# Kernel tuning notes

Hardware: AMD Instinct MI355X
Metric: run time of the kernel (lower is better)

## Reference

```python
import jax, jax.numpy as jnp
import numpy as np

H = 16      # n_heads
DK = 64     # d_k = d_v = input_dim // n_heads
D = 1024    # input_dim = ouput_dim


def setup_inputs() -> dict:
    key = jax.random.key(0)
    ks = jax.random.split(key, 10)
    s = 1.0 / np.float32(np.sqrt(D))
    inp = {
        'X':  jax.random.normal(ks[0], (2048, D), jnp.float32),
        'X1': jax.random.normal(ks[1], (3072, D), jnp.float32),
        'WQ':  jax.random.normal(ks[2], (D, H * DK), jnp.float32) * s,
        'WK':  jax.random.normal(ks[3], (D, H * DK), jnp.float32) * s,
        'WV':  jax.random.normal(ks[4], (D, H * DK), jnp.float32) * s,
        'WQ1': jax.random.normal(ks[5], (D, H * DK), jnp.float32) * s,
        'WK1': jax.random.normal(ks[6], (D, H * DK), jnp.float32) * s,
        'WV1': jax.random.normal(ks[7], (D, H * DK), jnp.float32) * s,
        'Wfc':  jax.random.normal(ks[8], (H * DK, D), jnp.float32) * s,
        'Wfc1': jax.random.normal(ks[9], (H * DK, D), jnp.float32) * s,
    }
    return inp


def _heads(x):
    # [N, H*DK] -> [H, N, DK]  (matches .view(-1,H,DK).transpose(0,1))
    return x.reshape(-1, H, DK).transpose(1, 0, 2)


def reference(X, X1, WQ, WK, WV, WQ1, WK1, WV1, Wfc, Wfc1):
    scale = jnp.float32(1.0 / np.sqrt(DK))
    Q,  K,  V  = _heads(X @ WQ),  _heads(X @ WK),  _heads(X @ WV)   # [H,N,DK]
    Q1, K1, V1 = _heads(X1 @ WQ1), _heads(X1 @ WK1), _heads(X1 @ WV1)  # [H,N1,DK]

    # direction 1: queries from X1 attend over X
    scores = jnp.einsum('hqd,hkd->hqk', Q1, K) * scale           # [H,N1,N]
    attn = jax.nn.softmax(scores, axis=-1)
    context = jnp.einsum('hqk,hkd->hqd', attn, V)                # [H,N1,DK]

    # direction 2: queries from X attend over X1
    scores1 = jnp.einsum('hqd,hkd->hqk', Q, K1) * scale          # [H,N,N1]
    attn1 = jax.nn.softmax(scores1, axis=-1)
    context1 = jnp.einsum('hqk,hkd->hqd', attn1, V1)             # [H,N,DK]

    # faithful to torch: .transpose(1,2).reshape(-1, H*DK) (head/len axes interleaved)
    context = context.transpose(0, 2, 1).reshape(-1, H * DK)     # [N1, H*DK] rows
    context1 = context1.transpose(0, 2, 1).reshape(-1, H * DK)   # [N,  H*DK] rows

    output = context @ Wfc     # [N1, D]
    output1 = context1 @ Wfc1  # [N,  D]
    return (output, output1)
```

## Files before the change

kernel.cpp:

```cpp
#include <hip/hip_runtime.h>
#include <stdint.h>

typedef unsigned short u16;
typedef unsigned int u32;
typedef u16   u16x4  __attribute__((ext_vector_type(4)));
typedef u16   u16x8  __attribute__((ext_vector_type(8)));
typedef short s16x4  __attribute__((ext_vector_type(4)));
typedef __bf16 bf16x4 __attribute__((ext_vector_type(4)));
typedef __bf16 bf16x8 __attribute__((ext_vector_type(8)));
typedef float f32x4  __attribute__((ext_vector_type(4)));
typedef u32   u32x2  __attribute__((ext_vector_type(2)));

typedef __attribute__((address_space(3))) u16 lds_u16;
typedef __attribute__((address_space(1))) const u16 glb_u16;

static __device__ __forceinline__ u16 f32_bf16(float f) {
    uint32_t u = __builtin_bit_cast(uint32_t, f);
    u += 0x7fffu + ((u >> 16) & 1u);
    return (u16)(u >> 16);
}
static __device__ __forceinline__ u32 pack_bf16(float a, float b) {
    return (u32)f32_bf16(a) | ((u32)f32_bf16(b) << 16);
}
static __device__ __forceinline__ u16x8 cvt8(f32x4 a, f32x4 b) {
    u16x8 v;
#pragma unroll
    for (int e = 0; e < 4; ++e) { v[e] = f32_bf16(a[e]); v[4 + e] = f32_bf16(b[e]); }
    return v;
}

static __device__ __forceinline__ f32x4 mfma16(u32x2 a, u32x2 b, f32x4 c) {
#if __has_builtin(__builtin_amdgcn_mfma_f32_16x16x16_bf16)
    return __builtin_amdgcn_mfma_f32_16x16x16_bf16(
        __builtin_bit_cast(bf16x4, a), __builtin_bit_cast(bf16x4, b), c, 0, 0, 0);
#elif __has_builtin(__builtin_amdgcn_mfma_f32_16x16x16bf16_1k)
    return __builtin_amdgcn_mfma_f32_16x16x16bf16_1k(
        __builtin_bit_cast(s16x4, a), __builtin_bit_cast(s16x4, b), c, 0, 0, 0);
#else
    f32x4 d;
    asm volatile("v_mfma_f32_16x16x16_bf16 %0, %1, %2, %3"
                 : "=v"(d) : "v"(a), "v"(b), "v"(c));
    return d;
#endif
}

__global__ __launch_bounds__(256) void detect_k(const u16* __restrict__ X, uint32_t* flag) {
    __shared__ int cnt[256];
    int t = threadIdx.x;
    int c = 0;
#pragma unroll
    for (int i = 0; i < 4; ++i) {
        u16 v = X[t + 256 * i];
        int e = (v >> 7) & 0xFF;
        c += (e >= 0xC2) ? 1 : 0;
    }
    cnt[t] = c;
    __syncthreads();
    for (int s = 128; s > 0; s >>= 1) {
        if (t < s) cnt[t] += cnt[t + s];
        __syncthreads();
    }
    if (t == 0) *flag = (cnt[0] > 32) ? 1u : 0u;
}

struct XJob { const void* in; u16* out; int n; };

__global__ __launch_bounds__(256) void convert_x(XJob j0, XJob j1, const uint32_t* __restrict__ flag) {
    const XJob job = (blockIdx.y == 0) ? j0 : j1;
    const bool f32in = (*flag != 0u);
    const int stride = gridDim.x * 256 * 8;
    for (int i = ((int)blockIdx.x * 256 + (int)threadIdx.x) * 8; i < job.n; i += stride) {
        u16x8 v;
        if (f32in) {
            const float* p = (const float*)job.in + i;
            v = cvt8(*(const f32x4*)p, *(const f32x4*)(p + 4));
        } else {
            v = *(const u16x8*)((const u16*)job.in + i);
        }
        *(u16x8*)(job.out + i) = v;
    }
}

struct WJob { const void* in; u16* out; };
struct WBatch8 { WJob j[8]; };

__global__ __launch_bounds__(256) void convert_w(WBatch8 args, const uint32_t* __restrict__ flag) {
    __shared__ u16 tile[64][72];
    const bool f32in = (*flag != 0u);
    const void* in = args.j[blockIdx.z].in;
    u16*       out = args.j[blockIdx.z].out;
    const int t  = threadIdx.x;
    const int r0 = blockIdx.y * 64, c0 = blockIdx.x * 64;
    const int lr = t >> 3, lc = (t & 7) * 8;
#pragma unroll
    for (int pass = 0; pass < 2; ++pass) {
        int r = lr + pass * 32;
        u16x8 v;
        if (f32in) {
            const float* p = (const float*)in + (size_t)(r0 + r) * 1024 + c0 + lc;
            v = cvt8(*(const f32x4*)p, *(const f32x4*)(p + 4));
        } else {
            v = *(const u16x8*)((const u16*)in + (size_t)(r0 + r) * 1024 + c0 + lc);
        }
#pragma unroll
        for (int e = 0; e < 8; ++e) tile[r][lc + e] = v[e];
    }
    __syncthreads();
#pragma unroll
    for (int pass = 0; pass < 2; ++pass) {
        int n = lr + pass * 32;
        u16x8 v;
#pragma unroll
        for (int e = 0; e < 8; ++e) v[e] = tile[lc + e][n];
        *(u16x8*)(out + (size_t)(c0 + n) * 1024 + r0 + lc) = v;
    }
}

struct GemmJob  { const u16* A; const u16* Bt; void* C; int M; int cF32able; int cOffElems; int vtNk; };
struct GemmBatch6 { GemmJob j[6]; };

__global__ __launch_bounds__(256) void gemm_bt(GemmBatch6 b, const uint32_t* __restrict__ flag) {
    const GemmJob job = b.j[blockIdx.z];
    const int K = 1024, N = 1024;
    const int m0 = blockIdx.y * 128;
    if (m0 >= job.M) return;
    const int n0 = blockIdx.x * 128;
    const bool cF = job.cF32able && (*flag != 0u);

    __shared__ u16 As[128 * 64];
    __shared__ u16 Bs[128 * 64];

    const int tid  = threadIdx.x;
    const int lane = tid & 63, wave = tid >> 6;
    const int quad = lane >> 4, l16 = lane & 15;
    const int wrow = wave >> 1, wcol = wave & 1;

    f32x4 acc[4][4];
#pragma unroll
    for (int i = 0; i < 4; ++i)
#pragma unroll
        for (int j = 0; j < 4; ++j) acc[i][j] = (f32x4){0.f, 0.f, 0.f, 0.f};

    for (int k0 = 0; k0 < K; k0 += 64) {
        __syncthreads();
#pragma unroll
        for (int i = 0; i < 4; ++i) {
            int id = tid + 256 * i;
            int row = id >> 3, slot = id & 7;
            int src = (slot ^ (row & 7)) * 8;
            __builtin_amdgcn_global_load_lds(
                (glb_u16*)(job.A + (size_t)(m0 + row) * K + k0 + src),
                (lds_u16*)(As + (size_t)id * 8), 16, 0, 0);
            __builtin_amdgcn_global_load_lds(
                (glb_u16*)(job.Bt + (size_t)(n0 + row) * K + k0 + src),
                (lds_u16*)(Bs + (size_t)id * 8), 16, 0, 0);
        }
        __syncthreads();

#pragma unroll
        for (int kc2 = 0; kc2 < 2; ++kc2) {
            bf16x8 af[4], bfb[4];
#pragma unroll
            for (int i = 0; i < 4; ++i) {
                int r  = wrow * 64 + i * 16 + l16;
                af[i]  = *(const bf16x8*)(As + r * 64 + (((kc2 * 4 + quad) ^ (r & 7)) * 8));
                int rn = wcol * 64 + i * 16 + l16;
                bfb[i] = *(const bf16x8*)(Bs + rn * 64 + (((kc2 * 4 + quad) ^ (rn & 7)) * 8));
            }
#pragma unroll
            for (int i = 0; i < 4; ++i)
#pragma unroll
                for (int j = 0; j < 4; ++j)
                    acc[i][j] = __builtin_amdgcn_mfma_f32_16x16x32_bf16(af[i], bfb[j], acc[i][j], 0, 0, 0);
        }
    }

    if (job.vtNk > 0) {
        u16* VT = (u16*)job.C;
        const int Nk2 = job.vtNk;
#pragma unroll
        for (int i = 0; i < 4; ++i)
#pragma unroll
            for (int j = 0; j < 4; ++j) {
                int n   = n0 + wcol * 64 + j * 16 + l16;
                int hh  = n >> 6, dd = n & 63;
                int key = m0 + wrow * 64 + i * 16 + quad * 4;
                u16x4 vv;
#pragma unroll
                for (int r = 0; r < 4; ++r) vv[r] = f32_bf16(acc[i][j][r]);
                *(u16x4*)(VT + (size_t)hh * 64 * Nk2 + (size_t)dd * Nk2 + key) = vv;
            }
    } else if (cF) {
        float* C = (float*)job.C + job.cOffElems;
#pragma unroll
        for (int i = 0; i < 4; ++i)
#pragma unroll
            for (int j = 0; j < 4; ++j)
#pragma unroll
                for (int r = 0; r < 4; ++r) {
                    int gr = m0 + wrow * 64 + i * 16 + quad * 4 + r;
                    int gc = n0 + wcol * 64 + j * 16 + l16;
                    C[(size_t)gr * N + gc] = acc[i][j][r];
                }
    } else {
        u16* C = (u16*)job.C + job.cOffElems;
#pragma unroll
        for (int i = 0; i < 4; ++i)
#pragma unroll
            for (int j = 0; j < 4; ++j)
#pragma unroll
                for (int r = 0; r < 4; ++r) {
                    int gr = m0 + wrow * 64 + i * 16 + quad * 4 + r;
                    int gc = n0 + wcol * 64 + j * 16 + l16;
                    C[(size_t)gr * N + gc] = f32_bf16(acc[i][j][r]);
                }
    }
}

struct AttnDir { const u16* Q; const u16* K; const u16* VT; u16* ctxT; int Nq; int Nk; int nBlk; };

__global__ __launch_bounds__(256, 4) void attn_k(AttnDir d0, AttnDir d1) {
    const int D = 1024;
    int b = blockIdx.x;
    const AttnDir dd = (b < d0.nBlk) ? d0 : d1;
    if (blockIdx.x >= (unsigned)d0.nBlk) b -= d0.nBlk;
    const int h  = b & 15;
    const int q0 = (b >> 4) * 64;
    const int Nq = dd.Nq, Nk = dd.Nk;
    const u16* __restrict__ Qp  = dd.Q;
    const u16* __restrict__ Kp  = dd.K;
    const u16* __restrict__ VTp = dd.VT;

    const int tid  = threadIdx.x;
    const int lane = tid & 63, w = tid >> 6;
    const int quad = lane >> 4, l16 = lane & 15;
    const int qhalf = w & 1, khalf = w >> 1;
    const int halfN = Nk >> 1;

    __shared__ u16 smem[18560];
    u16* Ks = smem + w * 4608;
    u16* Vs = Ks + 2048;
    float* Lb = (float*)(smem + 18432);

    bf16x8 aq[2][2];
#pragma unroll
    for (int ms = 0; ms < 2; ++ms)
#pragma unroll
        for (int kc = 0; kc < 2; ++kc) {
            int q = q0 + qhalf * 32 + ms * 16 + l16;
            aq[ms][kc] = *(const bf16x8*)(Qp + (size_t)q * D + h * 64 + kc * 32 + quad * 8);
        }

    f32x4 o[2][4];
#pragma unroll
    for (int ms = 0; ms < 2; ++ms)
#pragma unroll
        for (int nj = 0; nj < 4; ++nj) o[ms][nj] = (f32x4){0.f, 0.f, 0.f, 0.f};
    float rs[2] = {0.f, 0.f};
    const float sc = 0.125f;
    const size_t vtBase = (size_t)h * 64 * Nk;
    const int gkBase0 = khalf * halfN;

    int krow[4], ksrc[4], vd[4], vc[4];
#pragma unroll
    for (int i = 0; i < 4; ++i) {
        int id = i * 64 + lane;
        krow[i] = id >> 3;
        ksrc[i] = ((id & 7) ^ (krow[i] & 7)) * 8;
        vd[i]   = id >> 2;
        vc[i]   = id & 3;
    }

    u16x8 kr[4], vr[4];
#pragma unroll
    for (int i = 0; i < 4; ++i) {
        kr[i] = *(const u16x8*)(Kp + (size_t)(gkBase0 + krow[i]) * D + h * 64 + ksrc[i]);
        vr[i] = *(const u16x8*)(VTp + vtBase + (size_t)vd[i] * Nk + gkBase0 + vc[i] * 8);
    }

    for (int k0 = 0; k0 < halfN; k0 += 32) {
#pragma unroll
        for (int i = 0; i < 4; ++i) {
            *(u16x8*)(Ks + (i * 64 + lane) * 8) = kr[i];
            *(u16x8*)(Vs + vd[i] * 40 + vc[i] * 8) = vr[i];
        }
        {
            int kn = (k0 + 32 < halfN) ? (k0 + 32) : 0;
            int gkb = gkBase0 + kn;
#pragma unroll
            for (int i = 0; i < 4; ++i) {
                kr[i] = *(const u16x8*)(Kp + (size_t)(gkb + krow[i]) * D + h * 64 + ksrc[i]);
                vr[i] = *(const u16x8*)(VTp + vtBase + (size_t)vd[i] * Nk + gkb + vc[i] * 8);
            }
        }

        f32x4 s[2][2];
#pragma unroll
        for (int ms = 0; ms < 2; ++ms)
#pragma unroll
            for (int kn = 0; kn < 2; ++kn) s[ms][kn] = (f32x4){0.f, 0.f, 0.f, 0.f};
#pragma unroll
        for (int kn = 0; kn < 2; ++kn)
#pragma unroll
            for (int kc = 0; kc < 2; ++kc) {
                int keyr = kn * 16 + l16;
                int phys = ((kc * 4 + quad) ^ (keyr & 7)) * 8;
                bf16x8 ak = *(const bf16x8*)(Ks + keyr * 64 + phys);
#pragma unroll
                for (int ms = 0; ms < 2; ++ms)
                    s[ms][kn] = __builtin_amdgcn_mfma_f32_16x16x32_bf16(ak, aq[ms][kc], s[ms][kn], 0, 0, 0);
            }

        u32x2 pb[2][2];
#pragma unroll
        for (int ms = 0; ms < 2; ++ms)
#pragma unroll
            for (int kn = 0; kn < 2; ++kn) {
                float p0 = __expf(s[ms][kn][0] * sc);
                float p1 = __expf(s[ms][kn][1] * sc);
                float p2 = __expf(s[ms][kn][2] * sc);
                float p3 = __expf(s[ms][kn][3] * sc);
                rs[ms] += (p0 + p1) + (p2 + p3);
                pb[ms][kn][0] = pack_bf16(p0, p1);
                pb[ms][kn][1] = pack_bf16(p2, p3);
            }

#pragma unroll
        for (int nj = 0; nj < 4; ++nj) {
            int d = nj * 16 + l16;
#pragma unroll
            for (int kn = 0; kn < 2; ++kn) {
                u32x2 va = *(const u32x2*)(Vs + d * 40 + kn * 16 + quad * 4);
#pragma unroll
                for (int ms = 0; ms < 2; ++ms)
                    o[ms][nj] = mfma16(va, pb[ms][kn], o[ms][nj]);
            }
        }
    }

#pragma unroll
    for (int ms = 0; ms < 2; ++ms) {
        float v = rs[ms];
        v += __shfl_xor(v, 16, 64);
        v += __shfl_xor(v, 32, 64);
        rs[ms] = v;
    }

    __syncthreads();
    float* Cb = (float*)smem;
    if (khalf == 1) {
#pragma unroll
        for (int ms = 0; ms < 2; ++ms) {
            int ql = qhalf * 32 + ms * 16 + l16;
#pragma unroll
            for (int nj = 0; nj < 4; ++nj)
#pragma unroll
                for (int r = 0; r < 4; ++r)
                    Cb[ql * 65 + nj * 16 + quad * 4 + r] = o[ms][nj][r];
        }
        if (lane < 16) {
#pragma unroll
            for (int ms = 0; ms < 2; ++ms)
                Lb[qhalf * 32 + ms * 16 + l16] = rs[ms];
        }
    }
    __syncthreads();
    if (khalf == 0) {
#pragma unroll
        for (int ms = 0; ms < 2; ++ms) {
            int ql = qhalf * 32 + ms * 16 + l16;
            float inv = 1.0f / (rs[ms] + Lb[ql]);
            int q = q0 + ql;
#pragma unroll
            for (int nj = 0; nj < 4; ++nj)
#pragma unroll
                for (int r = 0; r < 4; ++r) {
                    int d = nj * 16 + quad * 4 + r;
                    float v = (o[ms][nj][r] + Cb[ql * 65 + d]) * inv;
                    dd.ctxT[(size_t)(h * 64 + d) * Nq + q] = f32_bf16(v);
                }
        }
    }
}

extern "C" void kernel_launch(void* const* d_in, const int* in_sizes, int n_in,
                              void* d_out, int out_size, void* d_ws, size_t ws_size,
                              hipStream_t stream) {
    u16* ws = (u16*)d_ws;
    uint32_t* flag = (uint32_t*)ws;
    u16* A = ws + 64;
    const size_t M1 = 1024ull * 1024;

    u16* W8   = A;
    u16* Kd1  = A + 8 * M1;
    u16* VT   = A + 10 * M1;
    u16* K1d  = A + 12 * M1;
    u16* VT1  = A + 15 * M1;
    u16* ctx2 = A + 18 * M1;

    u16* outw = (u16*)d_out;
    u16* Q1s  = outw;
    u16* Qs   = outw + 3 * M1;
    u16* Xb   = outw + 5 * M1;
    u16* X1b  = outw + 7 * M1;

    u16* ctx1 = W8;
    u16* WfcT = W8 + 6 * M1;

    detect_k<<<dim3(1), dim3(256), 0, stream>>>((const u16*)d_in[0], flag);

    XJob xj0 = {d_in[0], Xb,  2048 * 1024};
    XJob xj1 = {d_in[1], X1b, 3072 * 1024};
    convert_x<<<dim3(128, 2), dim3(256), 0, stream>>>(xj0, xj1, flag);

    WBatch8 wb;
    for (int i = 0; i < 8; ++i) { wb.j[i].in = d_in[2 + i]; wb.j[i].out = W8 + (size_t)i * M1; }
    convert_w<<<dim3(16, 16, 8), dim3(256), 0, stream>>>(wb, flag);

    GemmBatch6 gp;
    gp.j[0] = (GemmJob){Xb,  W8,          Qs,  2048, 0, 0, 0};
    gp.j[1] = (GemmJob){Xb,  W8 + M1,     Kd1, 2048, 0, 0, 0};
    gp.j[2] = (GemmJob){Xb,  W8 + 2 * M1, VT,  2048, 0, 0, 2048};
    gp.j[3] = (GemmJob){X1b, W8 + 3 * M1, Q1s, 3072, 0, 0, 0};
    gp.j[4] = (GemmJob){X1b, W8 + 4 * M1, K1d, 3072, 0, 0, 0};
    gp.j[5] = (GemmJob){X1b, W8 + 5 * M1, VT1, 3072, 0, 0, 3072};
    gemm_bt<<<dim3(8, 24, 6), dim3(256), 0, stream>>>(gp, flag);

    AttnDir a0 = {Qs,  K1d, VT1, ctx2, 2048, 3072, 512};
    AttnDir a1 = {Q1s, Kd1, VT,  ctx1, 3072, 2048, 768};
    attn_k<<<dim3(1280), dim3(256), 0, stream>>>(a0, a1);

    GemmBatch6 gf;
    gf.j[0] = (GemmJob){ctx1, WfcT,      d_out, 3072, 1, 0,               0};
    gf.j[1] = (GemmJob){ctx2, WfcT + M1, d_out, 2048, 1, 3 * 1024 * 1024, 0};
    gf.j[2] = gf.j[0]; gf.j[3] = gf.j[0]; gf.j[4] = gf.j[0]; gf.j[5] = gf.j[0];
    gemm_bt<<<dim3(8, 24, 2), dim3(256), 0, stream>>>(gf, flag);
}
```

Baseline: 291.3 us.

## Fold softmax scale into Q projection, use exp2, permute V layout for wider loads

Folds the 1/sqrt(dk)*log2(e) scale into the Q projection epilogue so the attention inner loop can call a raw exp2 instead of a multiply plus __expf. Packs the probabilities to bf16 with a byte-permute and round-half-up instead of the full round-to-nearest-even sequence. Reorders the key index inside each 32-key block when writing V transposed, so each lane fetches its V operands for both key halves with one 128-bit LDS read instead of two 64-bit reads. This trims VALU and LDS instructions in the attention loop, at the cost of slightly different rounding of Q and of the probabilities.

```diff
diff --git a/kernel.cpp b/kernel.cpp
--- a/kernel.cpp
+++ b/kernel.cpp
@@ -10,6 +10,7 @@
 typedef __bf16 bf16x8 __attribute__((ext_vector_type(8)));
 typedef float f32x4  __attribute__((ext_vector_type(4)));
 typedef u32   u32x2  __attribute__((ext_vector_type(2)));
+typedef u32   u32x4  __attribute__((ext_vector_type(4)));
 
 typedef __attribute__((address_space(3))) u16 lds_u16;
 typedef __attribute__((address_space(1))) const u16 glb_u16;
@@ -19,9 +20,20 @@
     u += 0x7fffu + ((u >> 16) & 1u);
     return (u16)(u >> 16);
 }
-static __device__ __forceinline__ u32 pack_bf16(float a, float b) {
+static __device__ __forceinline__ u32 pack2(float a, float b) {
+#if __has_builtin(__builtin_amdgcn_perm)
+    u32 ua = __builtin_bit_cast(u32, a) + 0x8000u;
+    u32 ub = __builtin_bit_cast(u32, b) + 0x8000u;
+    return __builtin_amdgcn_perm(ub, ua, 0x07060302u);
+#else
     return (u32)f32_bf16(a) | ((u32)f32_bf16(b) << 16);
-}
+#endif
+}
+#if __has_builtin(__builtin_amdgcn_exp2f)
+#define EXP2(x) __builtin_amdgcn_exp2f(x)
+#else
+#define EXP2(x) __expf((x) * 0.69314718056f)
+#endif
 static __device__ __forceinline__ u16x8 cvt8(f32x4 a, f32x4 b) {
     u16x8 v;
 #pragma unroll
@@ -116,7 +128,7 @@
     }
 }
 
-struct GemmJob  { const u16* A; const u16* Bt; void* C; int M; int cF32able; int cOffElems; int vtNk; };
+struct GemmJob  { const u16* A; const u16* Bt; void* C; int M; int cF32able; int cOffElems; int vtNk; float cScale; };
 struct GemmBatch6 { GemmJob j[6]; };
 
 __global__ __launch_bounds__(256) void gemm_bt(GemmBatch6 b, const uint32_t* __restrict__ flag) {
@@ -185,10 +197,12 @@
                 int n   = n0 + wcol * 64 + j * 16 + l16;
                 int hh  = n >> 6, dd = n & 63;
                 int key = m0 + wrow * 64 + i * 16 + quad * 4;
+                int bq  = key & 31;
+                int kp  = (key & ~31) | (((bq >> 2) & 3) * 8 + (bq >> 4) * 4);
                 u16x4 vv;
 #pragma unroll
                 for (int r = 0; r < 4; ++r) vv[r] = f32_bf16(acc[i][j][r]);
-                *(u16x4*)(VT + (size_t)hh * 64 * Nk2 + (size_t)dd * Nk2 + key) = vv;
+                *(u16x4*)(VT + (size_t)hh * 64 * Nk2 + (size_t)dd * Nk2 + kp) = vv;
             }
     } else if (cF) {
         float* C = (float*)job.C + job.cOffElems;
@@ -204,6 +218,7 @@
                 }
     } else {
         u16* C = (u16*)job.C + job.cOffElems;
+        const float cs = job.cScale;
 #pragma unroll
         for (int i = 0; i < 4; ++i)
 #pragma unroll
@@ -212,7 +227,7 @@
                 for (int r = 0; r < 4; ++r) {
                     int gr = m0 + wrow * 64 + i * 16 + quad * 4 + r;
                     int gc = n0 + wcol * 64 + j * 16 + l16;
-                    C[(size_t)gr * N + gc] = f32_bf16(acc[i][j][r]);
+                    C[(size_t)gr * N + gc] = f32_bf16(acc[i][j][r] * cs);
                 }
     }
 }
@@ -257,7 +272,6 @@
 #pragma unroll
         for (int nj = 0; nj < 4; ++nj) o[ms][nj] = (f32x4){0.f, 0.f, 0.f, 0.f};
     float rs[2] = {0.f, 0.f};
-    const float sc = 0.125f;
     const size_t vtBase = (size_t)h * 64 * Nk;
     const int gkBase0 = khalf * halfN;
 
@@ -316,24 +330,24 @@
         for (int ms = 0; ms < 2; ++ms)
 #pragma unroll
             for (int kn = 0; kn < 2; ++kn) {
-                float p0 = __expf(s[ms][kn][0] * sc);
-                float p1 = __expf(s[ms][kn][1] * sc);
-                float p2 = __expf(s[ms][kn][2] * sc);
-                float p3 = __expf(s[ms][kn][3] * sc);
+                float p0 = EXP2(s[ms][kn][0]);
+                float p1 = EXP2(s[ms][kn][1]);
+                float p2 = EXP2(s[ms][kn][2]);
+                float p3 = EXP2(s[ms][kn][3]);
                 rs[ms] += (p0 + p1) + (p2 + p3);
-                pb[ms][kn][0] = pack_bf16(p0, p1);
-                pb[ms][kn][1] = pack_bf16(p2, p3);
+                pb[ms][kn][0] = pack2(p0, p1);
+                pb[ms][kn][1] = pack2(p2, p3);
             }
 
 #pragma unroll
         for (int nj = 0; nj < 4; ++nj) {
             int d = nj * 16 + l16;
-#pragma unroll
-            for (int kn = 0; kn < 2; ++kn) {
-                u32x2 va = *(const u32x2*)(Vs + d * 40 + kn * 16 + quad * 4);
-#pragma unroll
-                for (int ms = 0; ms < 2; ++ms)
-                    o[ms][nj] = mfma16(va, pb[ms][kn], o[ms][nj]);
+            u32x4 va = *(const u32x4*)(Vs + d * 40 + quad * 8);
+            u32x2 va0 = {va[0], va[1]}, va1 = {va[2], va[3]};
+#pragma unroll
+            for (int ms = 0; ms < 2; ++ms) {
+                o[ms][nj] = mfma16(va0, pb[ms][0], o[ms][nj]);
+                o[ms][nj] = mfma16(va1, pb[ms][1], o[ms][nj]);
             }
         }
     }
@@ -390,6 +404,7 @@
     uint32_t* flag = (uint32_t*)ws;
     u16* A = ws + 64;
     const size_t M1 = 1024ull * 1024;
+    const float QSC = 0.125f * 1.44269504089f;
 
     u16* W8   = A;
     u16* Kd1  = A + 8 * M1;
@@ -418,12 +433,12 @@
     convert_w<<<dim3(16, 16, 8), dim3(256), 0, stream>>>(wb, flag);
 
     GemmBatch6 gp;
-    gp.j[0] = (GemmJob){Xb,  W8,          Qs,  2048, 0, 0, 0};
-    gp.j[1] = (GemmJob){Xb,  W8 + M1,     Kd1, 2048, 0, 0, 0};
-    gp.j[2] = (GemmJob){Xb,  W8 + 2 * M1, VT,  2048, 0, 0, 2048};
-    gp.j[3] = (GemmJob){X1b, W8 + 3 * M1, Q1s, 3072, 0, 0, 0};
-    gp.j[4] = (GemmJob){X1b, W8 + 4 * M1, K1d, 3072, 0, 0, 0};
-    gp.j[5] = (GemmJob){X1b, W8 + 5 * M1, VT1, 3072, 0, 0, 3072};
+    gp.j[0] = (GemmJob){Xb,  W8,          Qs,  2048, 0, 0, 0,    QSC};
+    gp.j[1] = (GemmJob){Xb,  W8 + M1,     Kd1, 2048, 0, 0, 0,    1.0f};
+    gp.j[2] = (GemmJob){Xb,  W8 + 2 * M1, VT,  2048, 0, 0, 2048, 1.0f};
+    gp.j[3] = (GemmJob){X1b, W8 + 3 * M1, Q1s, 3072, 0, 0, 0,    QSC};
+    gp.j[4] = (GemmJob){X1b, W8 + 4 * M1, K1d, 3072, 0, 0, 0,    1.0f};
+    gp.j[5] = (GemmJob){X1b, W8 + 5 * M1, VT1, 3072, 0, 0, 3072, 1.0f};
     gemm_bt<<<dim3(8, 24, 6), dim3(256), 0, stream>>>(gp, flag);
 
     AttnDir a0 = {Qs,  K1d, VT1, ctx2, 2048, 3072, 512};
@@ -431,8 +446,8 @@
     attn_k<<<dim3(1280), dim3(256), 0, stream>>>(a0, a1);
 
     GemmBatch6 gf;
-    gf.j[0] = (GemmJob){ctx1, WfcT,      d_out, 3072, 1, 0,               0};
-    gf.j[1] = (GemmJob){ctx2, WfcT + M1, d_out, 2048, 1, 3 * 1024 * 1024, 0};
+    gf.j[0] = (GemmJob){ctx1, WfcT,      d_out, 3072, 1, 0,               0, 1.0f};
+    gf.j[1] = (GemmJob){ctx2, WfcT + M1, d_out, 2048, 1, 3 * 1024 * 1024, 0, 1.0f};
     gf.j[2] = gf.j[0]; gf.j[3] = gf.j[0]; gf.j[4] = gf.j[0]; gf.j[5] = gf.j[0];
     gemm_bt<<<dim3(8, 24, 2), dim3(256), 0, stream>>>(gf, flag);
 }
```

Result: no change. 290.3 us (-0.4%).
